# Kernel optimization log

Hardware: AMD Instinct MI355X
Metric: run time of the kernel (lower is better)

Reference implementation:

```python
import jax, jax.numpy as jnp
import numpy as np

B, H, W, C = 4, 256, 256, 16
NT = 9


def _rot2(a):
    c, s = np.cos(a), np.sin(a)
    return np.array([[c, -s], [s, c]])


def _aff(m2):
    p = np.eye(3)
    p[:2, :2] = m2
    return p


def _t(tx, ty):
    p = np.eye(3)
    p[0, 2] = tx
    p[1, 2] = ty
    return p


def _refl(direction):
    # reflection across line through origin spanned by `direction`
    v = np.asarray(direction, dtype=np.float64)
    m2 = 2.0 * np.outer(v, v) / np.dot(v, v) - np.eye(2)
    return _aff(m2)


def _get_transforms(t0, t1, t2):
    L = np.eye(3)
    L[:2, 0] = t1
    L[:2, 1] = t2
    L[:2, 2] = t0
    rot = lambda n: _aff(_rot2(2.0 * np.pi / n))
    e = np.eye(3)
    r2 = _t(.5, .5) @ rot(2) @ _t(-.5, -.5)
    r3 = _t(.5, .5) @ rot(3) @ _t(-.5, -.5)
    r4 = _t(.5, .5) @ rot(4) @ _t(-.5, -.5)
    r6 = _t(.5, .5) @ rot(6) @ _t(-.5, -.5)
    f_p = _t(0, .5) @ np.diag([1.0, -1.0, 1.0]) @ _t(0, -.5)
    f_c = np.array([[0.0, 1, 0], [1, 0, 0], [0, 0, 1]])
    f_l = _t(.5, .5) @ _refl(_rot2(5 * np.pi / 6) @ np.array([1.0, 0.0])) @ _t(-.5, -.5)
    f_s = _t(.5, .5) @ _refl(_rot2(np.pi / 3) @ np.array([1.0, 0.0])) @ _t(-.5, -.5)
    Ts = np.stack([e, r2, r3, r4, r6, f_p, f_c, f_l, f_s])
    Ts = L[None] @ Ts @ np.linalg.inv(L)[None]
    Ts = np.linalg.inv(Ts)
    Ts = Ts / Ts[:, 2:3, 2:3]  # normalize so last entry is 1
    return Ts.reshape(NT, 9)[:, :8].astype(np.float32)  # TF flat transform params


def setup_inputs() -> dict:
    key = jax.random.key(0)
    inputs = jax.random.normal(key, (B, H, W, C), dtype=jnp.float32)
    transforms = jnp.asarray(_get_transforms((0.0, 0.0), (float(H), 0.0), (0.0, float(W))))
    return {"inputs": inputs, "transforms": transforms}


def _warp_nearest(img, flat):
    # TF image_projective_transform_v2 semantics with NEAREST interpolation,
    # constant (zero) fill. flat maps OUTPUT (x,y) -> INPUT (x,y).
    b, h, w, c = img.shape
    yy, xx = jnp.meshgrid(jnp.arange(h, dtype=jnp.float32),
                          jnp.arange(w, dtype=jnp.float32), indexing="ij")
    a0, a1, a2, a3, a4, a5, a6, a7 = [flat[i] for i in range(8)]
    k = a6 * xx + a7 * yy + 1.0
    xi = jnp.round((a0 * xx + a1 * yy + a2) / k).astype(jnp.int32)
    yi = jnp.round((a3 * xx + a4 * yy + a5) / k).astype(jnp.int32)
    valid = (xi >= 0) & (xi < w) & (yi >= 0) & (yi < h)
    xi = jnp.clip(xi, 0, w - 1)
    yi = jnp.clip(yi, 0, h - 1)
    out = img[:, yi, xi, :]  # [b,h,w,c] gather
    return jnp.where(valid[None, :, :, None], out, 0.0)


def _forward(inputs, transforms):
    b, h, w, c = inputs.shape
    nt = transforms.shape[0]
    # warp the input by each of the nt group transforms: [nt,b,h,w,c]
    yw = jax.vmap(lambda m: _warp_nearest(inputs, m))(transforms)
    x = jnp.broadcast_to(inputs[None], yw.shape)
    x = jnp.transpose(x, (0, 1, 4, 2, 3))   # [nt,b,c,h,w]
    yw = jnp.transpose(yw, (0, 1, 4, 2, 3))
    # circular normalized cross-correlation via FFT, per channel image
    fx = jnp.fft.rfft2(x)
    fy = jnp.fft.rfft2(yw)
    corr = jnp.fft.irfft2(fx * jnp.conj(fy), s=(h, w))  # [nt,b,c,h,w]
    nx = jnp.linalg.norm(x.reshape(nt, b, c, -1), axis=-1)[..., None, None]
    ny = jnp.linalg.norm(yw.reshape(nt, b, c, -1), axis=-1)[..., None, None]
    corr = corr / (nx * ny + 1e-12)
    out = corr.mean(axis=2)                  # mean over channels -> [nt,b,h,w]
    return jnp.transpose(out, (1, 2, 3, 0))  # channels_last [b,h,w,nt]


def reference(inputs, transforms):
    return _forward(inputs, transforms)
```

## Files before the change

kernel.cpp:

```cpp
#include <hip/hip_runtime.h>
#include <hip/hip_fp16.h>

#define Bn  4
#define Hn  256
#define Wn  256
#define Cn  16
#define NTn 9
#define HWn (Hn*Wn)
#define KF  129
#define KGP 136
#define SRL 266
#define PI_F 3.14159265358979323846f

__device__ __forceinline__ int swz(int i) { return i ^ ((i >> 4) & 15); }

__device__ __forceinline__ void lds_fence() {
  __asm__ volatile("s_waitcnt lgkmcnt(0)" ::: "memory");
}

__device__ __forceinline__ float2 cmul(float2 a, float2 b) {
  float2 r = make_float2(a.x, a.x) * b;
  return r + make_float2(-a.y, a.y) * make_float2(b.y, b.x);
}

template<bool INV>
__device__ __forceinline__ void radix4(float2& x0, float2& x1, float2& x2, float2& x3) {
  float2 y0 = x0 + x2;
  float2 y1 = x0 - x2;
  float2 y2 = x1 + x3;
  float2 y3 = x1 - x3;
  float2 j3 = INV ? make_float2(-y3.y, y3.x) : make_float2(y3.y, -y3.x);
  x0 = y0 + y2;
  x2 = y0 - y2;
  x1 = y1 + j3;
  x3 = y1 - j3;
}

struct Tw { float2 a1,a2,a3,b1,b2,b3,c1,c2,c3; };

template<bool INV>
__device__ __forceinline__ Tw make_tw(int lane) {
  const float sgn = INV ? 2.0f * PI_F : -2.0f * PI_F;
  Tw t; float sw, cw;
  __sincosf(sgn * (float)lane / 256.0f, &sw, &cw);
  t.a1 = make_float2(cw, sw); t.a2 = cmul(t.a1, t.a1); t.a3 = cmul(t.a2, t.a1);
  __sincosf(sgn * (float)(lane & 15) / 64.0f, &sw, &cw);
  t.b1 = make_float2(cw, sw); t.b2 = cmul(t.b1, t.b1); t.b3 = cmul(t.b2, t.b1);
  __sincosf(sgn * (float)(lane & 3) / 16.0f, &sw, &cw);
  t.c1 = make_float2(cw, sw); t.c2 = cmul(t.c1, t.c1); t.c3 = cmul(t.c2, t.c1);
  return t;
}

template<bool INV, int NF>
__device__ __forceinline__ void fft256_n(float2 (*v)[4], float2 (*s)[SRL],
                                         int lane, const Tw& t) {
#pragma unroll
  for (int f = 0; f < NF; ++f) {
    radix4<INV>(v[f][0], v[f][1], v[f][2], v[f][3]);
    v[f][1] = cmul(v[f][1], t.a1); v[f][2] = cmul(v[f][2], t.a2); v[f][3] = cmul(v[f][3], t.a3);
#pragma unroll
    for (int a = 0; a < 4; ++a) s[f][swz(lane + (a << 6))] = v[f][a];
  }
  lds_fence();
  { int base = (lane >> 4) * 64 + (lane & 15);
#pragma unroll
    for (int f = 0; f < NF; ++f)
#pragma unroll
      for (int a = 0; a < 4; ++a) v[f][a] = s[f][swz(base + (a << 4))];
  }
  lds_fence();
#pragma unroll
  for (int f = 0; f < NF; ++f) {
    radix4<INV>(v[f][0], v[f][1], v[f][2], v[f][3]);
    v[f][1] = cmul(v[f][1], t.b1); v[f][2] = cmul(v[f][2], t.b2); v[f][3] = cmul(v[f][3], t.b3);
    int base = (lane >> 4) * 64 + (lane & 15);
#pragma unroll
    for (int a = 0; a < 4; ++a) s[f][swz(base + (a << 4))] = v[f][a];
  }
  lds_fence();
  { int base = (lane >> 4) * 64 + ((lane >> 2) & 3) * 16 + (lane & 3);
#pragma unroll
    for (int f = 0; f < NF; ++f)
#pragma unroll
      for (int a = 0; a < 4; ++a) v[f][a] = s[f][swz(base + (a << 2))];
  }
  lds_fence();
#pragma unroll
  for (int f = 0; f < NF; ++f) {
    radix4<INV>(v[f][0], v[f][1], v[f][2], v[f][3]);
    v[f][1] = cmul(v[f][1], t.c1); v[f][2] = cmul(v[f][2], t.c2); v[f][3] = cmul(v[f][3], t.c3);
    int base = (lane & ~3) * 4 + (lane & 3);
#pragma unroll
    for (int a = 0; a < 4; ++a) s[f][swz(base + (a << 2))] = v[f][a];
  }
  lds_fence();
  { int base = lane * 4;
#pragma unroll
    for (int f = 0; f < NF; ++f)
#pragma unroll
      for (int a = 0; a < 4; ++a) v[f][a] = s[f][swz(base + a)];
  }
  lds_fence();
  int dr = ((lane & 3) << 4) + (((lane >> 2) & 3) << 2) + (lane >> 4);
#pragma unroll
  for (int f = 0; f < NF; ++f) {
    radix4<INV>(v[f][0], v[f][1], v[f][2], v[f][3]);
#pragma unroll
    for (int a = 0; a < 4; ++a) s[f][swz(dr + (a << 6))] = v[f][a];
  }
  lds_fence();
}

__device__ __forceinline__ int warp_id2(float a0, float a2, float a3, float a5,
                                        float a6, float p1, float p4, float p7,
                                        bool affine, int col) {
#pragma clang fp contract(off)
  float x = (float)col;
  float xf = (a0 * x + p1) + a2;
  float yf = (a3 * x + p4) + a5;
  if (!affine) {
    float kk = (a6 * x + p7) + 1.0f;
    xf = xf / kk;
    yf = yf / kk;
  }
  float xr = rintf(xf), yr = rintf(yf);
  bool valid = (xr >= 0.f) && (xr < 256.f) && (yr >= 0.f) && (yr < 256.f);
  return valid ? ((int)yr * Wn + (int)xr) : -1;
}

__global__ __launch_bounds__(256) void k_yrow(const float* __restrict__ inp,
                                              const float* __restrict__ T,
                                              __half2* __restrict__ Yh,
                                              float* __restrict__ part) {
  __shared__ float2 sb[4][4][SRL];
  __shared__ float4 redw[4];
  int tid = threadIdx.x, w = tid >> 6, lane = tid & 63;
  Tw t = make_tw<false>(lane);
  int chunk = blockIdx.x & 15, cg = (blockIdx.x >> 4) & 3, tb = blockIdx.x >> 6;
  int b = tb & 3, tt = tb >> 2;
  int i0 = chunk << 4;
  const float4* ib = (const float4*)(inp + (size_t)b * HWn * Cn);
  float a0, a1, a2, a3, a4, a5, a6, a7;
  { const float* a = T + tt * 8;
    a0=a[0]; a1=a[1]; a2=a[2]; a3=a[3]; a4=a[4]; a5=a[5]; a6=a[6]; a7=a[7]; }
  const bool affine = (fabsf(a6) + fabsf(a7)) * 255.0f < 2.9e-8f;
  float4 nyacc = make_float4(0.f, 0.f, 0.f, 0.f);

  auto store_half = [&](int h) {
    int ii = tid & 7, kq = tid >> 3;
    int w2 = ii >> 1, odd = ii & 1;
#pragma unroll
    for (int p = 0; p < 5; ++p) {
      int k = p * 32 + kq;
      if (k <= 128) {
        int kc = (256 - k) & 255;
#pragma unroll
        for (int cc = 0; cc < 4; ++cc) {
          float2 Z  = sb[w2][cc][swz(k)];
          float2 Zc = sb[w2][cc][swz(kc)];
          float2 F = odd ? make_float2(0.5f * (Z.y + Zc.y), 0.5f * (Zc.x - Z.x))
                         : make_float2(0.5f * (Z.x + Zc.x), 0.5f * (Z.y - Zc.y));
          Yh[((size_t)(tb * Cn + cg * 4 + cc) * KF + k) * Hn + i0 + h * 8 + ii] =
              __float22half2_rn(F);
        }
      }
    }
  };

  {
    int r0 = i0 + 2 * w;
    float yA = (float)r0, yB = (float)(r0 + 1);
    float p1A = a1 * yA, p4A = a4 * yA, p7A = a7 * yA;
    float p1B = a1 * yB, p4B = a4 * yB, p7B = a7 * yB;
    float4 g0[4], g1[4];
#pragma unroll
    for (int q = 0; q < 4; ++q) {
      int col = lane + (q << 6);
      int id0 = warp_id2(a0, a2, a3, a5, a6, p1A, p4A, p7A, affine, col);
      int id1 = warp_id2(a0, a2, a3, a5, a6, p1B, p4B, p7B, affine, col);
      g0[q] = (id0 >= 0) ? ib[(size_t)id0 * 4 + cg] : make_float4(0.f,0.f,0.f,0.f);
      g1[q] = (id1 >= 0) ? ib[(size_t)id1 * 4 + cg] : make_float4(0.f,0.f,0.f,0.f);
      nyacc += g0[q] * g0[q] + g1[q] * g1[q];
    }
    float2 v[4][4];
#pragma unroll
    for (int q = 0; q < 4; ++q) {
      v[0][q] = make_float2(g0[q].x, g1[q].x);
      v[1][q] = make_float2(g0[q].y, g1[q].y);
      v[2][q] = make_float2(g0[q].z, g1[q].z);
      v[3][q] = make_float2(g0[q].w, g1[q].w);
    }
    fft256_n<false, 4>(v, sb[w], lane, t);
  }
  __syncthreads();

  float4 G0[4], G1[4];
  {
    int r1 = i0 + 8 + 2 * w;
    float yA = (float)r1, yB = (float)(r1 + 1);
    float p1A = a1 * yA, p4A = a4 * yA, p7A = a7 * yA;
    float p1B = a1 * yB, p4B = a4 * yB, p7B = a7 * yB;
#pragma unroll
    for (int q = 0; q < 4; ++q) {
      int col = lane + (q << 6);
      int id0 = warp_id2(a0, a2, a3, a5, a6, p1A, p4A, p7A, affine, col);
      int id1 = warp_id2(a0, a2, a3, a5, a6, p1B, p4B, p7B, affine, col);
      G0[q] = (id0 >= 0) ? ib[(size_t)id0 * 4 + cg] : make_float4(0.f,0.f,0.f,0.f);
      G1[q] = (id1 >= 0) ? ib[(size_t)id1 * 4 + cg] : make_float4(0.f,0.f,0.f,0.f);
    }
  }

  store_half(0);
  __syncthreads();

  {
#pragma unroll
    for (int q = 0; q < 4; ++q)
      nyacc += G0[q] * G0[q] + G1[q] * G1[q];
    float2 v[4][4];
#pragma unroll
    for (int q = 0; q < 4; ++q) {
      v[0][q] = make_float2(G0[q].x, G1[q].x);
      v[1][q] = make_float2(G0[q].y, G1[q].y);
      v[2][q] = make_float2(G0[q].z, G1[q].z);
      v[3][q] = make_float2(G0[q].w, G1[q].w);
    }
    fft256_n<false, 4>(v, sb[w], lane, t);
  }
  __syncthreads();
  store_half(1);

#pragma unroll
  for (int o = 32; o > 0; o >>= 1) {
    nyacc.x += __shfl_down(nyacc.x, o, 64);
    nyacc.y += __shfl_down(nyacc.y, o, 64);
    nyacc.z += __shfl_down(nyacc.z, o, 64);
    nyacc.w += __shfl_down(nyacc.w, o, 64);
  }
  if (lane == 0) redw[w] = nyacc;
  __syncthreads();
  if (tid == 0) {
    float4 s = make_float4(redw[0].x + redw[1].x + redw[2].x + redw[3].x,
                           redw[0].y + redw[1].y + redw[2].y + redw[3].y,
                           redw[0].z + redw[1].z + redw[2].z + redw[3].z,
                           redw[0].w + redw[1].w + redw[2].w + redw[3].w);
    part[((size_t)tb * Cn + cg * 4 + 0) * 16 + chunk] = s.x;
    part[((size_t)tb * Cn + cg * 4 + 1) * 16 + chunk] = s.y;
    part[((size_t)tb * Cn + cg * 4 + 2) * 16 + chunk] = s.z;
    part[((size_t)tb * Cn + cg * 4 + 3) * 16 + chunk] = s.w;
  }
}

__global__ __launch_bounds__(256) void k_colfft_fx(const __half2* __restrict__ Yh,
                                                   __half2* __restrict__ Fxh) {
  __shared__ float2 sb[4][4][SRL];
  int tid = threadIdx.x, w = tid >> 6, lane = tid & 63;
  Tw t = make_tw<false>(lane);
  int base_item = blockIdx.x * 16 + w * 4;
  float2 v[4][4];
#pragma unroll
  for (int f = 0; f < 4; ++f) {
    const __half2* Sp = Yh + (size_t)(base_item + f) * Hn;
#pragma unroll
    for (int q = 0; q < 4; ++q) v[f][q] = __half22float2(Sp[lane + (q << 6)]);
  }
  fft256_n<false, 4>(v, sb[w], lane, t);
#pragma unroll
  for (int f = 0; f < 4; ++f) {
    __half2* Op = Fxh + (size_t)(base_item + f) * Hn;
#pragma unroll
    for (int q = 0; q < 4; ++q) {
      int j = lane + (q << 6);
      Op[j] = __float22half2_rn(sb[w][f][swz(j)]);
    }
  }
}

__global__ __launch_bounds__(256) void k_ycol(const __half2* __restrict__ Yh,
                                              const __half2* __restrict__ Fxh,
                                              const float* __restrict__ part,
                                              float2* __restrict__ G) {
  __shared__ float2 sb[4][2][SRL];
  __shared__ float scs[16];
  int tid = threadIdx.x, w = tid >> 6, lane = tid & 63;
  int tb = blockIdx.x / 33, quart = blockIdx.x % 33;
  int b = tb & 3;
  if (tid < 16) {
    float sx = 0.f, sy = 0.f;
#pragma unroll
    for (int ch = 0; ch < 16; ++ch) {
      sx += part[((size_t)b  * Cn + tid) * 16 + ch];
      sy += part[((size_t)tb * Cn + tid) * 16 + ch];
    }
    scs[tid] = 1.0f / ((float)Cn * (sqrtf(sx) * sqrtf(sy) + 1e-12f));
  }
  __syncthreads();
  int k = quart * 4 + w;
  bool act = (k <= 128);
  if (act) {
    Tw tf = make_tw<false>(lane);
    float2 acc[4];
#pragma unroll
    for (int q = 0; q < 4; ++q) acc[q] = make_float2(0.f, 0.f);
    for (int c = 0; c < Cn; c += 2) {
      float2 v2[2][4];
#pragma unroll
      for (int e = 0; e < 2; ++e) {
        const __half2* Yp = Yh + ((size_t)(tb * Cn + c + e) * KF + k) * Hn;
#pragma unroll
        for (int q = 0; q < 4; ++q) v2[e][q] = __half22float2(Yp[lane + (q << 6)]);
      }
      fft256_n<false, 2>(v2, sb[w], lane, tf);
#pragma unroll
      for (int e = 0; e < 2; ++e) {
        float sc = scs[c + e];
        const __half2* Fxp = Fxh + ((size_t)(b * Cn + c + e) * KF + k) * Hn;
#pragma unroll
        for (int q = 0; q < 4; ++q) {
          int rr = lane + (q << 6);
          float2 fy = sb[w][e][swz(rr)];
          float2 fx = __half22float2(Fxp[rr]);
          float2 pr = make_float2(fy.x, fy.x) * fx
                    + make_float2(fy.y, fy.y) * make_float2(fx.y, -fx.x);
          acc[q] += make_float2(sc, sc) * pr;
        }
      }
    }
    Tw ti = make_tw<true>(lane);
    fft256_n<true, 1>(reinterpret_cast<float2(*)[4]>(acc), sb[w], lane, ti);
  }
  __syncthreads();
  int kk = tid & 3, jj0 = tid >> 2;
  if (quart * 4 + kk <= 128) {
    float2* Gp = G + ((size_t)tb * Hn) * KGP + quart * 4 + kk;
#pragma unroll
    for (int p = 0; p < 4; ++p) {
      int j = jj0 + (p << 6);
      Gp[(size_t)j * KGP] = sb[kk][0][swz(j)];
    }
  }
}

__global__ __launch_bounds__(320) void k_irow(const float2* __restrict__ G,
                                              float* __restrict__ out) {
  __shared__ float2 tile[5][2][132];
  __shared__ float2 sb[5][SRL];
  __shared__ float rowbuf[Wn * NTn];
  int tid = threadIdx.x, w = tid >> 6, lane = tid & 63;
  Tw ti = make_tw<true>(lane);
  int b = blockIdx.x >> 8, i = blockIdx.x & 255;
  const float scale = 1.0f / ((float)Hn * (float)Wn);
  int t1 = 2 * w, t2 = t1 + 1;
  {
    const float2* Gp1 = G + ((size_t)(t1 * Bn + b) * Hn + i) * KGP;
    for (int k = lane; k < KF; k += 64) tile[w][0][k] = Gp1[k];
    if (t2 < NTn) {
      const float2* Gp2 = G + ((size_t)(t2 * Bn + b) * Hn + i) * KGP;
      for (int k = lane; k < KF; k += 64) tile[w][1][k] = Gp2[k];
    }
  }
  lds_fence();
  float2 v[1][4];
#pragma unroll
  for (int q = 0; q < 4; ++q) {
    int k = lane + (q << 6);
    float2 a, bb;
    if (k <= 128) a = tile[w][0][k];
    else { float2 z = tile[w][0][256 - k]; a = make_float2(z.x, -z.y); }
    if (t2 < NTn) {
      if (k <= 128) bb = tile[w][1][k];
      else { float2 z = tile[w][1][256 - k]; bb = make_float2(z.x, -z.y); }
    } else bb = make_float2(0.f, 0.f);
    v[0][q] = a + make_float2(-bb.y, bb.x);
  }
  fft256_n<true, 1>(v, reinterpret_cast<float2(*)[SRL]>(sb[w]), lane, ti);
#pragma unroll
  for (int q = 0; q < 4; ++q) {
    int j = lane + (q << 6);
    float2 r = sb[w][swz(j)];
    rowbuf[j * NTn + t1] = r.x * scale;
    if (t2 < NTn) rowbuf[j * NTn + t2] = r.y * scale;
  }
  __syncthreads();
  float* ob = out + ((size_t)(b * Hn + i) * Wn) * NTn;
  for (int f = tid; f < Wn * NTn; f += 320) ob[f] = rowbuf[f];
}

extern "C" void kernel_launch(void* const* d_in, const int* in_sizes, int n_in,
                              void* d_out, int out_size, void* d_ws, size_t ws_size,
                              hipStream_t stream) {
  const float* inp = (const float*)d_in[0];
  const float* T   = (const float*)d_in[1];
  float* out = (float*)d_out;
  char* ws = (char*)d_ws;

  size_t off = 0;
  float*   part = (float*)(ws + off);  off += (size_t)NTn * Bn * Cn * 16 * sizeof(float);
  __half2* Fxh = (__half2*)(ws + off); off += (size_t)Bn * Cn * KF * Hn * sizeof(__half2);
  float2*  G   = (float2*)(ws + off);  off += (size_t)NTn * Bn * Hn * KGP * sizeof(float2);
  __half2* Yh  = (__half2*)(ws + off); off += (size_t)NTn * Bn * Cn * KF * Hn * sizeof(__half2);
  (void)off; (void)ws_size; (void)in_sizes; (void)n_in; (void)out_size;

  k_yrow<<<NTn * Bn * 64, 256, 0, stream>>>(inp, T, Yh, part);
  k_colfft_fx<<<Bn * Cn * KF / 4 / 4, 256, 0, stream>>>(Yh, Fxh);
  k_ycol<<<NTn * Bn * 33, 256, 0, stream>>>(Yh, Fxh, part, G);
  k_irow<<<Bn * Hn, 320, 0, stream>>>(G, out);
}
```

Measured before the change: 181.1 us.

## Batch four channels per column FFT with Y prefetch; drop explicit LDS waitcnt fences

The k_ycol kernel now runs column FFTs four channels at a time instead of two. It double-buffers register tiles so the next group's half-precision Y loads are issued while the current group's FFT and accumulation proceed, and the shared scratch is enlarged to match. Separately, the manual s_waitcnt lgkmcnt(0) fences inside the wave-local FFT and in k_irow are removed, leaving LDS ordering to the compiler's own waits. This costs far more registers, which may lower occupancy, and relies on in-order per-wave LDS semantics for correctness.

```diff
diff --git a/kernel.cpp b/kernel.cpp
--- a/kernel.cpp
+++ b/kernel.cpp
@@ -13,10 +13,6 @@
 #define PI_F 3.14159265358979323846f
 
 __device__ __forceinline__ int swz(int i) { return i ^ ((i >> 4) & 15); }
-
-__device__ __forceinline__ void lds_fence() {
-  __asm__ volatile("s_waitcnt lgkmcnt(0)" ::: "memory");
-}
 
 __device__ __forceinline__ float2 cmul(float2 a, float2 b) {
   float2 r = make_float2(a.x, a.x) * b;
@@ -61,14 +57,12 @@
 #pragma unroll
     for (int a = 0; a < 4; ++a) s[f][swz(lane + (a << 6))] = v[f][a];
   }
-  lds_fence();
   { int base = (lane >> 4) * 64 + (lane & 15);
 #pragma unroll
     for (int f = 0; f < NF; ++f)
 #pragma unroll
       for (int a = 0; a < 4; ++a) v[f][a] = s[f][swz(base + (a << 4))];
   }
-  lds_fence();
 #pragma unroll
   for (int f = 0; f < NF; ++f) {
     radix4<INV>(v[f][0], v[f][1], v[f][2], v[f][3]);
@@ -77,14 +71,12 @@
 #pragma unroll
     for (int a = 0; a < 4; ++a) s[f][swz(base + (a << 4))] = v[f][a];
   }
-  lds_fence();
   { int base = (lane >> 4) * 64 + ((lane >> 2) & 3) * 16 + (lane & 3);
 #pragma unroll
     for (int f = 0; f < NF; ++f)
 #pragma unroll
       for (int a = 0; a < 4; ++a) v[f][a] = s[f][swz(base + (a << 2))];
   }
-  lds_fence();
 #pragma unroll
   for (int f = 0; f < NF; ++f) {
     radix4<INV>(v[f][0], v[f][1], v[f][2], v[f][3]);
@@ -93,14 +85,12 @@
 #pragma unroll
     for (int a = 0; a < 4; ++a) s[f][swz(base + (a << 2))] = v[f][a];
   }
-  lds_fence();
   { int base = lane * 4;
 #pragma unroll
     for (int f = 0; f < NF; ++f)
 #pragma unroll
       for (int a = 0; a < 4; ++a) v[f][a] = s[f][swz(base + a)];
   }
-  lds_fence();
   int dr = ((lane & 3) << 4) + (((lane >> 2) & 3) << 2) + (lane >> 4);
 #pragma unroll
   for (int f = 0; f < NF; ++f) {
@@ -108,7 +98,6 @@
 #pragma unroll
     for (int a = 0; a < 4; ++a) s[f][swz(dr + (a << 6))] = v[f][a];
   }
-  lds_fence();
 }
 
 __device__ __forceinline__ int warp_id2(float a0, float a2, float a3, float a5,
@@ -280,7 +269,7 @@
                                               const __half2* __restrict__ Fxh,
                                               const float* __restrict__ part,
                                               float2* __restrict__ G) {
-  __shared__ float2 sb[4][2][SRL];
+  __shared__ float2 sb[4][4][SRL];
   __shared__ float scs[16];
   int tid = threadIdx.x, w = tid >> 6, lane = tid & 63;
   int tb = blockIdx.x / 33, quart = blockIdx.x % 33;
@@ -302,19 +291,23 @@
     float2 acc[4];
 #pragma unroll
     for (int q = 0; q < 4; ++q) acc[q] = make_float2(0.f, 0.f);
-    for (int c = 0; c < Cn; c += 2) {
-      float2 v2[2][4];
-#pragma unroll
-      for (int e = 0; e < 2; ++e) {
-        const __half2* Yp = Yh + ((size_t)(tb * Cn + c + e) * KF + k) * Hn;
-#pragma unroll
-        for (int q = 0; q < 4; ++q) v2[e][q] = __half22float2(Yp[lane + (q << 6)]);
+    const __half2* Ybase = Yh  + ((size_t)(tb * Cn) * KF + k) * Hn;
+    const __half2* Fbase = Fxh + ((size_t)(b  * Cn) * KF + k) * Hn;
+
+    float2 va[4][4], vb[4][4];
+    auto LOADY = [&](float2 (*v)[4], int c0) {
+#pragma unroll
+      for (int e = 0; e < 4; ++e) {
+        const __half2* Yp = Ybase + (size_t)(c0 + e) * KF * Hn;
+#pragma unroll
+        for (int q = 0; q < 4; ++q) v[e][q] = __half22float2(Yp[lane + (q << 6)]);
       }
-      fft256_n<false, 2>(v2, sb[w], lane, tf);
-#pragma unroll
-      for (int e = 0; e < 2; ++e) {
-        float sc = scs[c + e];
-        const __half2* Fxp = Fxh + ((size_t)(b * Cn + c + e) * KF + k) * Hn;
+    };
+    auto ACC = [&](int c0) {
+#pragma unroll
+      for (int e = 0; e < 4; ++e) {
+        float sc = scs[c0 + e];
+        const __half2* Fxp = Fbase + (size_t)(c0 + e) * KF * Hn;
 #pragma unroll
         for (int q = 0; q < 4; ++q) {
           int rr = lane + (q << 6);
@@ -325,7 +318,14 @@
           acc[q] += make_float2(sc, sc) * pr;
         }
       }
-    }
+    };
+
+    LOADY(va, 0);
+    fft256_n<false, 4>(va, sb[w], lane, tf);  LOADY(vb, 4);   ACC(0);
+    fft256_n<false, 4>(vb, sb[w], lane, tf);  LOADY(va, 8);   ACC(4);
+    fft256_n<false, 4>(va, sb[w], lane, tf);  LOADY(vb, 12);  ACC(8);
+    fft256_n<false, 4>(vb, sb[w], lane, tf);                  ACC(12);
+
     Tw ti = make_tw<true>(lane);
     fft256_n<true, 1>(reinterpret_cast<float2(*)[4]>(acc), sb[w], lane, ti);
   }
@@ -359,7 +359,6 @@
       for (int k = lane; k < KF; k += 64) tile[w][1][k] = Gp2[k];
     }
   }
-  lds_fence();
   float2 v[1][4];
 #pragma unroll
   for (int q = 0; q < 4; ++q) {
```

Measured after the change: 178.0 us. Within noise of the previous version (-1.7%).
